# Kernel tuning notes

Measured on AMD Instinct MI355X. Metric: run time of the kernel, lower is better.

## Reference

```python
import jax, jax.numpy as jnp
import numpy as np

B, S, HID = 2, 2048, 1024
H, D = 16, 64  # num query heads, head_dim; single shared KV head
SCALE = D ** -0.5


def setup_inputs() -> dict:
    key = jax.random.key(0)
    k1, k2, k3, k4, k5 = jax.random.split(key, 5)
    return {
        "hidden_states": jax.random.normal(k1, (B, S, HID), dtype=jnp.float32),
        "Wq": jax.random.normal(k2, (HID, HID), dtype=jnp.float32) * 0.02,
        "Wk": jax.random.normal(k3, (HID, D), dtype=jnp.float32) * 0.02,
        "Wv": jax.random.normal(k4, (HID, D), dtype=jnp.float32) * 0.02,
        "Wo": jax.random.normal(k5, (HID, HID), dtype=jnp.float32) * 0.02,
    }


def reference(hidden_states, Wq, Wk, Wv, Wo):
    b, s, _ = hidden_states.shape
    # projections: Q has H heads; K/V have a single shared head of dim D
    q = (hidden_states @ Wq).reshape(b, s, H, D)  # [B,S,H,D]
    k = hidden_states @ Wk                        # [B,S,D]
    v = hidden_states @ Wv                        # [B,S,D]
    # scores: broadcast single KV head across all query heads
    scores = jnp.einsum("bqhd,bkd->bhqk", q, k) * SCALE  # [B,H,S,S]
    attn = jax.nn.softmax(scores, axis=-1)
    out = jnp.einsum("bhqk,bkd->bqhd", attn, v).reshape(b, s, HID)
    return out @ Wo
```

## Files before the change

kernel.cpp:

```cpp
#include <hip/hip_runtime.h>
#include <math.h>

#define BATCH 2
#define SEQ   2048
#define HID   1024
#define NH    16
#define HD    64
#define MTOT  (BATCH * SEQ)

#define PST 72
#define WTS 69

#define EXP_C1 0.1803368801111255f
#define EXP_C2 (-17.312340490667562f)

typedef __attribute__((ext_vector_type(8))) short short8;
typedef __attribute__((ext_vector_type(4))) float floatx4;
typedef __attribute__((ext_vector_type(16))) float floatx16;
typedef __attribute__((ext_vector_type(4))) unsigned int uint4v;

#define MFMA32(a, b, c) __builtin_amdgcn_mfma_f32_32x32x16_bf16(a, b, c, 0, 0, 0)
#define MFMA16(a, b, c) __builtin_amdgcn_mfma_f32_16x16x32_bf16(a, b, c, 0, 0, 0)

static __device__ __forceinline__ floatx16 zero16() {
    floatx16 z;
    #pragma unroll
    for (int i = 0; i < 16; ++i) z[i] = 0.f;
    return z;
}

__device__ __forceinline__ unsigned short f2bf(float x) {
    unsigned u = __float_as_uint(x);
    u += 0x7FFF + ((u >> 16) & 1);
    return (unsigned short)(u >> 16);
}
__device__ __forceinline__ float bf2f(unsigned short h) {
    return __uint_as_float((unsigned)h << 16);
}
__device__ __forceinline__ void split16(const float* f, unsigned short* hh, unsigned short* ll) {
    #pragma unroll
    for (int e = 0; e < 16; ++e) {
        unsigned short h = f2bf(f[e]);
        hh[e] = h;
        ll[e] = f2bf(f[e] - bf2f(h));
    }
}

__device__ __forceinline__ void gld16(const unsigned short* g, unsigned short* l) {
    __builtin_amdgcn_global_load_lds(
        (const __attribute__((address_space(1))) unsigned int*)g,
        (__attribute__((address_space(3))) unsigned int*)l, 16, 0, 0);
}


__global__ __launch_bounds__(256)
void presplit_kernel(const float* __restrict__ Wq, const float* __restrict__ Wk,
                     const float* __restrict__ Wv, const float* __restrict__ Wo,
                     const float* __restrict__ X,
                     unsigned short* __restrict__ WqTh, unsigned short* __restrict__ WqTl,
                     unsigned short* __restrict__ WkTh, unsigned short* __restrict__ WkTl,
                     unsigned short* __restrict__ WvTh, unsigned short* __restrict__ WvTl,
                     unsigned short* __restrict__ WoTh, unsigned short* __restrict__ WoTl,
                     unsigned short* __restrict__ Xh)
{
    __shared__ __align__(16) float Wtmp[64][WTS];
    const int tid = threadIdx.x;
    int bx = blockIdx.x;

    if (bx >= 544) {
        size_t i0 = (size_t)(bx - 544) * 4096 + tid * 16;
        float f[16];
        *(float4*)&f[0]  = *(const float4*)(X + i0 + 0);
        *(float4*)&f[4]  = *(const float4*)(X + i0 + 4);
        *(float4*)&f[8]  = *(const float4*)(X + i0 + 8);
        *(float4*)&f[12] = *(const float4*)(X + i0 + 12);
        unsigned short hh[16];
        #pragma unroll
        for (int e = 0; e < 16; ++e) hh[e] = f2bf(f[e]);
        const int m  = (bx - 544) * 4 + (tid >> 6);
        const int k0 = (tid & 63) * 16;
        const int m32 = m >> 5, mi = (m >> 4) & 1, tr = m & 15;
        #pragma unroll
        for (int c = 0; c < 2; ++c) {
            const int k = k0 + c * 8;
            const int ktx = k >> 6, ksx = (k >> 5) & 1, qd = (k >> 3) & 3;
            size_t off = (((size_t)(m32 * 16 + ktx) * 2 + ksx) * 2 + mi) * 512
                       + (qd * 16 + tr) * 8;
            *(uint4*)(Xh + off) = *(uint4*)&hh[c * 8];
        }
        return;
    }

    const float* W; unsigned short *Th, *Tl; int ldw, kt, nt;
    if (bx < 256)      { W = Wq; Th = WqTh; Tl = WqTl; ldw = HID; kt = bx >> 4; nt = bx & 15; }
    else if (bx < 272) { W = Wk; Th = WkTh; Tl = WkTl; ldw = HD;  kt = bx - 256; nt = 0; }
    else if (bx < 288) { W = Wv; Th = WvTh; Tl = WvTl; ldw = HD;  kt = bx - 272; nt = 0; }
    else               { W = Wo; Th = WoTh; Tl = WoTl; ldw = HID; bx -= 288; kt = bx >> 4; nt = bx & 15; }
    const int k0 = kt * 64, n0 = nt * 64;

    {
        const int wk = tid >> 2, wn = (tid & 3) * 16;
        const float* wp = W + (size_t)(k0 + wk) * ldw + n0 + wn;
        float f[16];
        *(float4*)&f[0]  = *(const float4*)(wp + 0);
        *(float4*)&f[4]  = *(const float4*)(wp + 4);
        *(float4*)&f[8]  = *(const float4*)(wp + 8);
        *(float4*)&f[12] = *(const float4*)(wp + 12);
        #pragma unroll
        for (int e = 0; e < 16; ++e) Wtmp[wk][wn + e] = f[e];
    }
    __syncthreads();
    {
        const int rn = tid >> 2, rk = (tid & 3) * 16;
        float f[16];
        #pragma unroll
        for (int e = 0; e < 16; ++e) f[e] = Wtmp[rk + e][rn];
        unsigned short hh[16], ll[16];
        split16(f, hh, ll);
        const int sub = rn >> 4, tw = rn & 15;
        const size_t tb = ((size_t)nt * 16 + kt) * 4096;
        const int ksA = rk >> 5,       qA = (rk >> 3) & 3;
        const int ksB = (rk + 8) >> 5, qB = ((rk + 8) >> 3) & 3;
        const size_t offA = tb + (size_t)(ksA * 4 + sub) * 512 + (qA * 16 + tw) * 8;
        const size_t offB = tb + (size_t)(ksB * 4 + sub) * 512 + (qB * 16 + tw) * 8;
        *(uint4*)(Th + offA) = *(uint4*)&hh[0];
        *(uint4*)(Th + offB) = *(uint4*)&hh[8];
        *(uint4*)(Tl + offA) = *(uint4*)&ll[0];
        *(uint4*)(Tl + offB) = *(uint4*)&ll[8];
    }
}

__global__ __launch_bounds__(256)
void qkv_kernel(const unsigned short* __restrict__ Xfo,
                const unsigned short* __restrict__ WqTh, const unsigned short* __restrict__ WqTl,
                const unsigned short* __restrict__ WkTh, const unsigned short* __restrict__ WkTl,
                const unsigned short* __restrict__ WvTh, const unsigned short* __restrict__ WvTl,
                unsigned short* __restrict__ Qh,
                unsigned short* __restrict__ Kh, unsigned short* __restrict__ Vth)
{
    __shared__ __align__(16) unsigned short Wst[2][2][4096];

    const int tid  = threadIdx.x;
    const int wave = tid >> 6, lane = tid & 63;
    const int t = lane & 15, quad = lane >> 4;
    const int m0 = blockIdx.x * 128;
    const int nb = blockIdx.y;

    const unsigned short *WTh, *WTl; int nt;
    if (nb < 16)       { WTh = WqTh; WTl = WqTl; nt = nb; }
    else if (nb == 16) { WTh = WkTh; WTl = WkTl; nt = 0; }
    else               { WTh = WvTh; WTl = WvTl; nt = 0; }

    floatx4 acc[2][4];
    #pragma unroll
    for (int mi = 0; mi < 2; ++mi)
        #pragma unroll
        for (int sub = 0; sub < 4; ++sub) acc[mi][sub] = (floatx4){0.f,0.f,0.f,0.f};

    const size_t abase = ((size_t)(blockIdx.x * 4 + wave) * 16) * 2048 + lane * 8;
    const int g0 = wave * 2;

    auto STAGE = [&](int buf, int kt) {
        const size_t tb = ((size_t)nt * 16 + kt) * 4096 + g0 * 512 + lane * 8;
        gld16(WTh + tb,       &Wst[buf][0][g0 * 512]);
        gld16(WTh + tb + 512, &Wst[buf][0][g0 * 512 + 512]);
        gld16(WTl + tb,       &Wst[buf][1][g0 * 512]);
        gld16(WTl + tb + 512, &Wst[buf][1][g0 * 512 + 512]);
    };
    auto COMPUTE = [&](int buf, short8 a00, short8 a01, short8 a10, short8 a11) {
        #pragma unroll
        for (int ksq = 0; ksq < 2; ++ksq) {
            short8 am0 = ksq ? a10 : a00;
            short8 am1 = ksq ? a11 : a01;
            #pragma unroll
            for (int sub = 0; sub < 4; ++sub) {
                const int g = ksq * 4 + sub;
                short8 bh = *(const short8*)&Wst[buf][0][g * 512 + lane * 8];
                short8 bl = *(const short8*)&Wst[buf][1][g * 512 + lane * 8];
                acc[0][sub] = MFMA16(am0, bh, acc[0][sub]);
                acc[0][sub] = MFMA16(am0, bl, acc[0][sub]);
                acc[1][sub] = MFMA16(am1, bh, acc[1][sub]);
                acc[1][sub] = MFMA16(am1, bl, acc[1][sub]);
            }
        }
    };

    short8 a00, a01, a10, a11;
    {
        const unsigned short* ab = Xfo + abase;
        a00 = *(const short8*)(ab);
        a01 = *(const short8*)(ab + 512);
        a10 = *(const short8*)(ab + 1024);
        a11 = *(const short8*)(ab + 1536);
    }
    STAGE(0, 0);
    __syncthreads();

    int cur = 0;
    for (int kt = 0; kt < HID / 64 - 1; ++kt) {
        STAGE(cur ^ 1, kt + 1);
        const unsigned short* ab = Xfo + abase + (size_t)(kt + 1) * 2048;
        short8 n00 = *(const short8*)(ab);
        short8 n01 = *(const short8*)(ab + 512);
        short8 n10 = *(const short8*)(ab + 1024);
        short8 n11 = *(const short8*)(ab + 1536);

        COMPUTE(cur, a00, a01, a10, a11);

        __syncthreads();
        a00 = n00; a01 = n01; a10 = n10; a11 = n11;
        cur ^= 1;
    }
    COMPUTE(cur, a00, a01, a10, a11);

    #pragma unroll
    for (int mi = 0; mi < 2; ++mi)
        #pragma unroll
        for (int sub = 0; sub < 4; ++sub)
            #pragma unroll
            for (int r = 0; r < 4; ++r) {
                int g = m0 + wave * 32 + mi * 16 + quad * 4 + r;
                int d = sub * 16 + t;
                unsigned short hh = f2bf(acc[mi][sub][r]);
                if (nb < 16) {
                    int b = g >> 11, s = g & (SEQ - 1);
                    Qh[((size_t)(b * NH + nb) * SEQ + s) * HD + d] = hh;
                } else if (nb == 16) {
                    Kh[(size_t)g * HD + d] = hh;
                } else {
                    int b = g >> 11, s = g & (SEQ - 1);
                    Vth[(size_t)b * HD * SEQ + (size_t)d * SEQ + s] = hh;
                }
            }
}

__global__ __launch_bounds__(512, 4)
void flash_kernel(const unsigned short* __restrict__ Qhg,
                  const unsigned short* __restrict__ Khg,
                  const unsigned short* __restrict__ Vthg,
                  unsigned short* __restrict__ Oh)
{
    __shared__ __align__(16) char smem[33792];
    unsigned short (*Ksh)[PST] = (unsigned short (*)[PST])smem;
    unsigned short (*Vsh)[PST] = (unsigned short (*)[PST])(smem + 64 * PST * 2);

    const int tid  = threadIdx.x;
    const int wave = tid >> 6, lane = tid & 63;
    const int lq = lane & 31, hi = lane >> 5;
    const int qw = wave >> 1;
    const int ks = wave & 1;

    const int q0 = blockIdx.x * 128;
    const int h  = blockIdx.y;
    const int b  = blockIdx.z;

    short8 qreg[4];
    {
        const unsigned short* qp =
            Qhg + ((size_t)(b * NH + h) * SEQ + q0 + qw * 32 + lq) * HD + hi * 8;
        #pragma unroll
        for (int dc = 0; dc < 4; ++dc) qreg[dc] = *(const short8*)(qp + dc * 16);
    }

    const unsigned short* Kh_b  = Khg  + (size_t)b * SEQ * HD;
    const unsigned short* Vth_b = Vthg + (size_t)b * HD * SEQ;

    const int sr = tid >> 3, sc = (tid & 7) * 8;

    float l_part = 0.f;
    floatx16 o0 = zero16(), o1 = zero16();

    uint4 gk = *(const uint4*)(Kh_b + (size_t)sr * HD + sc);
    uint4 gv = *(const uint4*)(Vth_b + (size_t)sr * SEQ + sc);

    for (int kt = 0; kt < SEQ / 64; ++kt) {
        __syncthreads();
        *(uint4*)&Ksh[sr][sc] = gk;
        *(uint4*)&Vsh[sr][sc] = gv;
        if (kt + 1 < SEQ / 64) {
            gk = *(const uint4*)(Kh_b + (size_t)((kt + 1) * 64 + sr) * HD + sc);
            gv = *(const uint4*)(Vth_b + (size_t)sr * SEQ + (kt + 1) * 64 + sc);
        }
        __syncthreads();

        floatx16 sf = zero16();
        __builtin_amdgcn_s_setprio(1);
        #pragma unroll
        for (int dc = 0; dc < 4; ++dc) {
            short8 kf = *(const short8*)&Ksh[ks * 32 + lq][dc * 16 + hi * 8];
            sf = MFMA32(kf, qreg[dc], sf);
        }
        __builtin_amdgcn_s_setprio(0);

        unsigned w0[4], w1[4];
        #pragma unroll
        for (int rr = 0; rr < 4; ++rr) {
            unsigned u0 = __float_as_uint(exp2f(fmaf(sf[rr * 4 + 0], EXP_C1, EXP_C2)));
            unsigned u1 = __float_as_uint(exp2f(fmaf(sf[rr * 4 + 1], EXP_C1, EXP_C2)));
            unsigned u2 = __float_as_uint(exp2f(fmaf(sf[rr * 4 + 2], EXP_C1, EXP_C2)));
            unsigned u3 = __float_as_uint(exp2f(fmaf(sf[rr * 4 + 3], EXP_C1, EXP_C2)));
            l_part += __uint_as_float(u0 & 0xFFFF0000u) + __uint_as_float(u1 & 0xFFFF0000u)
                    + __uint_as_float(u2 & 0xFFFF0000u) + __uint_as_float(u3 & 0xFFFF0000u);
            w0[rr] = (u0 >> 16) | (u1 & 0xFFFF0000u);
            w1[rr] = (u2 >> 16) | (u3 & 0xFFFF0000u);
        }

        #pragma unroll
        for (int mm = 0; mm < 2; ++mm) {
            unsigned send0 = hi ? w0[2 * mm] : w0[2 * mm + 1];
            unsigned send1 = hi ? w1[2 * mm] : w1[2 * mm + 1];
            unsigned recv0 = (unsigned)__shfl_xor((int)send0, 32);
            unsigned recv1 = (unsigned)__shfl_xor((int)send1, 32);
            unsigned own0 = hi ? w0[2 * mm + 1] : w0[2 * mm];
            unsigned own1 = hi ? w1[2 * mm + 1] : w1[2 * mm];
            uint4v pw;
            pw.x = hi ? recv0 : own0;
            pw.y = hi ? recv1 : own1;
            pw.z = hi ? own0 : recv0;
            pw.w = hi ? own1 : recv1;
            short8 pa = __builtin_bit_cast(short8, pw);
            short8 v0 = *(const short8*)&Vsh[lq][ks * 32 + mm * 16 + hi * 8];
            short8 v1 = *(const short8*)&Vsh[32 + lq][ks * 32 + mm * 16 + hi * 8];
            __builtin_amdgcn_s_setprio(1);
            o0 = MFMA32(pa, v0, o0);
            o1 = MFMA32(pa, v1, o1);
            __builtin_amdgcn_s_setprio(0);
        }
    }

    float l_wave = l_part + __shfl_xor(l_part, 32);
    __syncthreads();
    float* cb = (float*)smem;
    const int cbase = (qw * 64 + lane) * 33;
    if (ks) {
        #pragma unroll
        for (int r = 0; r < 16; ++r) { cb[cbase + r] = o0[r]; cb[cbase + 16 + r] = o1[r]; }
        cb[cbase + 32] = l_wave;
    }
    __syncthreads();
    if (!ks) {
        float l_tot = l_wave + cb[cbase + 32];
        const int m32 = b * 64 + blockIdx.x * 4 + qw;
        #pragma unroll
        for (int r = 0; r < 16; ++r) {
            int qr = (r & 3) + 8 * (r >> 2) + 4 * hi;
            float inv = 1.0f / __shfl(l_tot, qr);
            float a0 = o0[r] + cb[cbase + r];
            float a1 = o1[r] + cb[cbase + 16 + r];
            int mi = qr >> 4, tr = qr & 15;
            size_t base = (((size_t)(m32 * 16 + h) * 2 + 0) * 2 + mi) * 512
                        + ((lq >> 3) * 16 + tr) * 8 + (lq & 7);
            Oh[base]        = f2bf(a0 * inv);
            Oh[base + 1024] = f2bf(a1 * inv);
        }
    }
}

__global__ __launch_bounds__(256)
void out_proj_kernel(const unsigned short* __restrict__ Ofo,
                     const unsigned short* __restrict__ WoTh,
                     const unsigned short* __restrict__ WoTl,
                     float* __restrict__ out)
{
    __shared__ __align__(16) unsigned short Wst[2][2][4096];

    const int tid  = threadIdx.x;
    const int wave = tid >> 6, lane = tid & 63;
    const int t = lane & 15, quad = lane >> 4;
    const int m0 = blockIdx.x * 128;
    const int nt = blockIdx.y;

    floatx4 acc[2][4];
    #pragma unroll
    for (int mi = 0; mi < 2; ++mi)
        #pragma unroll
        for (int sub = 0; sub < 4; ++sub) acc[mi][sub] = (floatx4){0.f,0.f,0.f,0.f};

    const size_t abase = ((size_t)(blockIdx.x * 4 + wave) * 16) * 2048 + lane * 8;
    const int g0 = wave * 2;

    auto STAGE = [&](int buf, int kt) {
        const size_t tb = ((size_t)nt * 16 + kt) * 4096 + g0 * 512 + lane * 8;
        gld16(WoTh + tb,       &Wst[buf][0][g0 * 512]);
        gld16(WoTh + tb + 512, &Wst[buf][0][g0 * 512 + 512]);
        gld16(WoTl + tb,       &Wst[buf][1][g0 * 512]);
        gld16(WoTl + tb + 512, &Wst[buf][1][g0 * 512 + 512]);
    };
    auto COMPUTE = [&](int buf, short8 a00, short8 a01, short8 a10, short8 a11) {
        #pragma unroll
        for (int ksq = 0; ksq < 2; ++ksq) {
            short8 am0 = ksq ? a10 : a00;
            short8 am1 = ksq ? a11 : a01;
            #pragma unroll
            for (int sub = 0; sub < 4; ++sub) {
                const int g = ksq * 4 + sub;
                short8 bh = *(const short8*)&Wst[buf][0][g * 512 + lane * 8];
                short8 bl = *(const short8*)&Wst[buf][1][g * 512 + lane * 8];
                acc[0][sub] = MFMA16(am0, bh, acc[0][sub]);
                acc[0][sub] = MFMA16(am0, bl, acc[0][sub]);
                acc[1][sub] = MFMA16(am1, bh, acc[1][sub]);
                acc[1][sub] = MFMA16(am1, bl, acc[1][sub]);
            }
        }
    };

    short8 a00, a01, a10, a11;
    {
        const unsigned short* ab = Ofo + abase;
        a00 = *(const short8*)(ab);
        a01 = *(const short8*)(ab + 512);
        a10 = *(const short8*)(ab + 1024);
        a11 = *(const short8*)(ab + 1536);
    }
    STAGE(0, 0);
    __syncthreads();

    int cur = 0;
    for (int kt = 0; kt < HID / 64 - 1; ++kt) {
        STAGE(cur ^ 1, kt + 1);
        const unsigned short* ab = Ofo + abase + (size_t)(kt + 1) * 2048;
        short8 n00 = *(const short8*)(ab);
        short8 n01 = *(const short8*)(ab + 512);
        short8 n10 = *(const short8*)(ab + 1024);
        short8 n11 = *(const short8*)(ab + 1536);

        COMPUTE(cur, a00, a01, a10, a11);

        __syncthreads();
        a00 = n00; a01 = n01; a10 = n10; a11 = n11;
        cur ^= 1;
    }
    COMPUTE(cur, a00, a01, a10, a11);

    const int n0 = nt * 64;
    #pragma unroll
    for (int mi = 0; mi < 2; ++mi)
        #pragma unroll
        for (int sub = 0; sub < 4; ++sub)
            #pragma unroll
            for (int r = 0; r < 4; ++r)
                out[(size_t)(m0 + wave * 32 + mi * 16 + quad * 4 + r) * HID
                    + n0 + sub * 16 + t] = acc[mi][sub][r];
}

extern "C" void kernel_launch(void* const* d_in, const int* in_sizes, int n_in,
                              void* d_out, int out_size, void* d_ws, size_t ws_size,
                              hipStream_t stream)
{
    const float* X  = (const float*)d_in[0];
    const float* Wq = (const float*)d_in[1];
    const float* Wk = (const float*)d_in[2];
    const float* Wv = (const float*)d_in[3];
    const float* Wo = (const float*)d_in[4];
    float* out = (float*)d_out;

    unsigned short* Qh = (unsigned short*)d_out;
    unsigned short* Xh = Qh + (size_t)BATCH * NH * SEQ * HD;

    char* ws = (char*)d_ws;
    const size_t SZ_WQ = (size_t)HID * HID * 2;
    const size_t SZ_WK = (size_t)HD * HID * 2;
    unsigned short* WqTh = (unsigned short*)(ws);
    unsigned short* WqTl = (unsigned short*)(ws + SZ_WQ);
    unsigned short* WkTh = (unsigned short*)(ws + 2*SZ_WQ);
    unsigned short* WkTl = (unsigned short*)(ws + 2*SZ_WQ + SZ_WK);
    unsigned short* WvTh = (unsigned short*)(ws + 2*SZ_WQ + 2*SZ_WK);
    unsigned short* WvTl = (unsigned short*)(ws + 2*SZ_WQ + 3*SZ_WK);
    unsigned short* WoTh = (unsigned short*)(ws + 2*SZ_WQ + 4*SZ_WK);
    unsigned short* WoTl = (unsigned short*)(ws + 3*SZ_WQ + 4*SZ_WK);
    unsigned short* Kh   = (unsigned short*)(ws + 4*SZ_WQ + 4*SZ_WK);
    unsigned short* Vth  = (unsigned short*)(ws + 4*SZ_WQ + 4*SZ_WK + (size_t)MTOT*HD*2);
    unsigned short* Oh   = (unsigned short*)(ws + 4*SZ_WQ + 4*SZ_WK + (size_t)MTOT*HD*4);

    presplit_kernel<<<dim3(1568), 256, 0, stream>>>(Wq, Wk, Wv, Wo, X,
        WqTh, WqTl, WkTh, WkTl, WvTh, WvTl, WoTh, WoTl, Xh);
    qkv_kernel<<<dim3(MTOT / 128, 18), 256, 0, stream>>>(Xh,
        WqTh, WqTl, WkTh, WkTl, WvTh, WvTl, Qh, Kh, Vth);
    flash_kernel<<<dim3(SEQ / 128, NH, BATCH), 512, 0, stream>>>(Qh, Kh, Vth, Oh);
    out_proj_kernel<<<dim3(MTOT / 128, HID / 64), 256, 0, stream>>>(Oh, WoTh, WoTl, out);
}
```

Baseline: 186.8 us.

## Fold softmax scale into Q, permute K rows, compute row sums via MFMA

Folds the exp2 scale constant into Q at projection time and drops the constant offset, so the softmax is a bare exp2 of the score. The K rows read from shared memory are permuted so each lane's score outputs already match the P operand layout for the PV MFMA, which removes the cross-half lane shuffles. Row sums now come from an extra MFMA against a ones vector instead of scalar adds and a final shuffle. The trade is one more MFMA per step, and removing the offset raises overflow risk for large scores.

```diff
diff --git a/kernel.cpp b/kernel.cpp
--- a/kernel.cpp
+++ b/kernel.cpp
@@ -12,7 +12,6 @@
 #define WTS 69
 
 #define EXP_C1 0.1803368801111255f
-#define EXP_C2 (-17.312340490667562f)
 
 typedef __attribute__((ext_vector_type(8))) short short8;
 typedef __attribute__((ext_vector_type(4))) float floatx4;
@@ -221,15 +220,15 @@
             for (int r = 0; r < 4; ++r) {
                 int g = m0 + wave * 32 + mi * 16 + quad * 4 + r;
                 int d = sub * 16 + t;
-                unsigned short hh = f2bf(acc[mi][sub][r]);
                 if (nb < 16) {
                     int b = g >> 11, s = g & (SEQ - 1);
-                    Qh[((size_t)(b * NH + nb) * SEQ + s) * HD + d] = hh;
+                    Qh[((size_t)(b * NH + nb) * SEQ + s) * HD + d] =
+                        f2bf(acc[mi][sub][r] * EXP_C1);
                 } else if (nb == 16) {
-                    Kh[(size_t)g * HD + d] = hh;
+                    Kh[(size_t)g * HD + d] = f2bf(acc[mi][sub][r]);
                 } else {
                     int b = g >> 11, s = g & (SEQ - 1);
-                    Vth[(size_t)b * HD * SEQ + (size_t)d * SEQ + s] = hh;
+                    Vth[(size_t)b * HD * SEQ + (size_t)d * SEQ + s] = f2bf(acc[mi][sub][r]);
                 }
             }
 }
@@ -249,6 +248,7 @@
     const int lq = lane & 31, hi = lane >> 5;
     const int qw = wave >> 1;
     const int ks = wave & 1;
+    const int klq = (lq & ~12) | ((lq & 4) << 1) | ((lq & 8) >> 1);
 
     const int q0 = blockIdx.x * 128;
     const int h  = blockIdx.y;
@@ -267,8 +267,10 @@
 
     const int sr = tid >> 3, sc = (tid & 7) * 8;
 
-    float l_part = 0.f;
-    floatx16 o0 = zero16(), o1 = zero16();
+    floatx16 o0 = zero16(), o1 = zero16(), ol = zero16();
+    short8 onesB;
+    #pragma unroll
+    for (int j = 0; j < 8; ++j) onesB[j] = (short)0x3F80;
 
     uint4 gk = *(const uint4*)(Kh_b + (size_t)sr * HD + sc);
     uint4 gv = *(const uint4*)(Vth_b + (size_t)sr * SEQ + sc);
@@ -287,64 +289,53 @@
         __builtin_amdgcn_s_setprio(1);
         #pragma unroll
         for (int dc = 0; dc < 4; ++dc) {
-            short8 kf = *(const short8*)&Ksh[ks * 32 + lq][dc * 16 + hi * 8];
+            short8 kf = *(const short8*)&Ksh[ks * 32 + klq][dc * 16 + hi * 8];
             sf = MFMA32(kf, qreg[dc], sf);
         }
         __builtin_amdgcn_s_setprio(0);
 
-        unsigned w0[4], w1[4];
-        #pragma unroll
-        for (int rr = 0; rr < 4; ++rr) {
-            unsigned u0 = __float_as_uint(exp2f(fmaf(sf[rr * 4 + 0], EXP_C1, EXP_C2)));
-            unsigned u1 = __float_as_uint(exp2f(fmaf(sf[rr * 4 + 1], EXP_C1, EXP_C2)));
-            unsigned u2 = __float_as_uint(exp2f(fmaf(sf[rr * 4 + 2], EXP_C1, EXP_C2)));
-            unsigned u3 = __float_as_uint(exp2f(fmaf(sf[rr * 4 + 3], EXP_C1, EXP_C2)));
-            l_part += __uint_as_float(u0 & 0xFFFF0000u) + __uint_as_float(u1 & 0xFFFF0000u)
-                    + __uint_as_float(u2 & 0xFFFF0000u) + __uint_as_float(u3 & 0xFFFF0000u);
-            w0[rr] = (u0 >> 16) | (u1 & 0xFFFF0000u);
-            w1[rr] = (u2 >> 16) | (u3 & 0xFFFF0000u);
-        }
-
         #pragma unroll
         for (int mm = 0; mm < 2; ++mm) {
-            unsigned send0 = hi ? w0[2 * mm] : w0[2 * mm + 1];
-            unsigned send1 = hi ? w1[2 * mm] : w1[2 * mm + 1];
-            unsigned recv0 = (unsigned)__shfl_xor((int)send0, 32);
-            unsigned recv1 = (unsigned)__shfl_xor((int)send1, 32);
-            unsigned own0 = hi ? w0[2 * mm + 1] : w0[2 * mm];
-            unsigned own1 = hi ? w1[2 * mm + 1] : w1[2 * mm];
+            unsigned uu[8];
+            #pragma unroll
+            for (int j = 0; j < 8; ++j)
+                uu[j] = __float_as_uint(exp2f(sf[mm * 8 + j]));
             uint4v pw;
-            pw.x = hi ? recv0 : own0;
-            pw.y = hi ? recv1 : own1;
-            pw.z = hi ? own0 : recv0;
-            pw.w = hi ? own1 : recv1;
+            pw.x = (uu[0] >> 16) | (uu[1] & 0xFFFF0000u);
+            pw.y = (uu[2] >> 16) | (uu[3] & 0xFFFF0000u);
+            pw.z = (uu[4] >> 16) | (uu[5] & 0xFFFF0000u);
+            pw.w = (uu[6] >> 16) | (uu[7] & 0xFFFF0000u);
             short8 pa = __builtin_bit_cast(short8, pw);
             short8 v0 = *(const short8*)&Vsh[lq][ks * 32 + mm * 16 + hi * 8];
             short8 v1 = *(const short8*)&Vsh[32 + lq][ks * 32 + mm * 16 + hi * 8];
             __builtin_amdgcn_s_setprio(1);
+            ol = MFMA32(pa, onesB, ol);
             o0 = MFMA32(pa, v0, o0);
             o1 = MFMA32(pa, v1, o1);
             __builtin_amdgcn_s_setprio(0);
         }
     }
 
-    float l_wave = l_part + __shfl_xor(l_part, 32);
     __syncthreads();
-    float* cb = (float*)smem;
-    const int cbase = (qw * 64 + lane) * 33;
+    float* cb  = (float*)smem;
+    float* cbl = (float*)(smem + 32768);
+    const int cbase = (qw * 64 + lane) * 32;
     if (ks) {
         #pragma unroll
         for (int r = 0; r < 16; ++r) { cb[cbase + r] = o0[r]; cb[cbase + 16 + r] = o1[r]; }
-        cb[cbase + 32] = l_wave;
+        if (lq == 0) {
+            #pragma unroll
+            for (int r = 0; r < 16; ++r) cbl[(qw * 2 + hi) * 16 + r] = ol[r];
+        }
     }
     __syncthreads();
     if (!ks) {
-        float l_tot = l_wave + cb[cbase + 32];
         const int m32 = b * 64 + blockIdx.x * 4 + qw;
         #pragma unroll
         for (int r = 0; r < 16; ++r) {
             int qr = (r & 3) + 8 * (r >> 2) + 4 * hi;
-            float inv = 1.0f / __shfl(l_tot, qr);
+            float ltot = ol[r] + cbl[(qw * 2 + hi) * 16 + r];
+            float inv = 1.0f / ltot;
             float a0 = o0[r] + cb[cbase + r];
             float a1 = o1[r] + cb[cbase + 16 + r];
             int mi = qr >> 4, tr = qr & 15;
```

After: 177.4 us. 1.05x faster.
